# Kernel optimization log

Hardware: AMD Instinct MI355X
Metric: run time of the kernel (lower is better)

Reference implementation:

```python
import jax, jax.numpy as jnp
import numpy as np
from jax import lax

B, L, M, K = 4096, 1000, 16, 20
PRIOR_LOC, PRIOR_SCALE = -0.01, 0.001


def _motif_probs(x, w):
    # x: [B,4,L], w: [M,4*K] -> sigmoid(max_t conv(x, w_m)) : [B,M]
    kern = w.reshape(M, 4, K)
    scores = lax.conv_general_dilated(x, kern, (1,), 'VALID',
                                      dimension_numbers=('NCH', 'OIH', 'NCH'))  # [B,M,L-K+1]
    return jax.nn.sigmoid(scores.max(-1))


def _z(x, w):
    # pz_wyx_network: Bernoulli(p).log_prob(0) + log_prob(1) per motif, then softmax over motifs
    p = _motif_probs(x, w)                    # [B,M]
    lp = jnp.log(p) + jnp.log1p(-p)
    return jax.nn.softmax(lp, axis=-1)


def _kl(q_loc, q_scale):
    # KL(N(q_loc,q_scale) || N(PRIOR_LOC, PRIOR_SCALE)), summed over all dims
    return (jnp.log(PRIOR_SCALE / q_scale)
            + (q_scale ** 2 + (q_loc - PRIOR_LOC) ** 2) / (2.0 * PRIOR_SCALE ** 2)
            - 0.5).sum()


def setup_inputs() -> dict:
    key = jax.random.key(0)
    ks = jax.random.split(key, 6)
    x = jax.random.uniform(ks[0], (B, 4, L), dtype=jnp.float32)
    y = (jax.random.uniform(ks[1], (B,)) > 0.5).astype(jnp.float32)
    qw_loc = jax.random.normal(ks[2], (M, 4 * K), dtype=jnp.float32)
    qw_scale_raw = jax.random.normal(ks[3], (M, 4 * K), dtype=jnp.float32)
    gen_scale = jnp.full((1,), -15.0, dtype=jnp.float32)
    eps1 = jax.random.normal(ks[4], (M, 4 * K), dtype=jnp.float32)
    eps2 = jax.random.normal(ks[5], (M, 4 * K), dtype=jnp.float32)
    return dict(x=x, y=y, qw_loc=qw_loc, qw_scale_raw=qw_scale_raw,
                gen_scale=gen_scale, eps1=eps1, eps2=eps2)


def reference(x, y, qw_loc, qw_scale_raw, gen_scale, eps1, eps2):
    q_scale = jax.nn.softplus(qw_scale_raw)
    # --- ELBO assembly (forward) ---
    w1 = qw_loc + q_scale * eps1              # first rsample
    z = _z(x, w1)                             # [B,M]
    elbo = (z * jnp.log(1e-20 + z)).sum(1)    # [B]
    elbo = elbo + 2.0 * _kl(qw_loc, q_scale)  # KL added twice in original forward
    w2 = qw_loc + q_scale * eps2              # second rsample
    p = _motif_probs(x, w2)                   # [B,M] generative_loc per motif
    s = 1.0 / jax.nn.softplus(gen_scale)[0]
    eps = 1e-16
    gll = -jnp.log(eps + (eps + p) ** s + (eps + 1.0 - p) ** s)          # [B,M]
    # BCELoss() has reduction='mean' -> scalar per motif (log clamped at -100 like torch)
    bce = -(y[:, None] * jnp.clip(jnp.log(p), -100.0)
            + (1.0 - y)[:, None] * jnp.clip(jnp.log(1.0 - p), -100.0)).mean(0)  # [M]
    gll = gll - s * bce[None, :]
    elbo = elbo - (z * gll).sum(1)
    loss = elbo.mean()
    # --- predict: per-sample gathered kernel conv (batched via grouped conv) ---
    assign = _z(x, qw_loc).argmax(-1)         # [B] motif assignment per sample
    w_z = qw_loc[assign].reshape(B, 4, K)     # gathered per-sample kernels
    xg = x.reshape(1, B * 4, L)
    sc = lax.conv_general_dilated(xg, w_z, (1,), 'VALID',
                                  dimension_numbers=('NCH', 'OIH', 'NCH'),
                                  feature_group_count=B)                # [1,B,L-K+1]
    y_pred = jax.nn.sigmoid(sc[0].max(-1))    # [B]
    return loss, y_pred
```

## Files before the change

kernel.cpp:

```cpp
#include <hip/hip_runtime.h>
#include <math.h>

#define B_N 4096
#define TVALID 981

typedef _Float16 f16x8 __attribute__((ext_vector_type(8)));
typedef float f32x16 __attribute__((ext_vector_type(16)));

#define WS_FRAG 0
#define WS_RED  5120

static __device__ __forceinline__ float softplus_f(float x) {
    return fmaxf(x, 0.f) + log1pf(expf(-fabsf(x)));
}
static __device__ __forceinline__ uint32_t pkh(_Float16 a, _Float16 b) {
    return (uint32_t)__builtin_bit_cast(unsigned short, a)
         | ((uint32_t)__builtin_bit_cast(unsigned short, b) << 16);
}
static __device__ __forceinline__ f16x8 mkfrag(uint32_t d0, uint32_t d1, uint32_t d2, uint32_t d3) {
    union { uint32_t u[4]; f16x8 v; } t;
    t.u[0] = d0; t.u[1] = d1; t.u[2] = d2; t.u[3] = d3;
    return t.v;
}

__global__ void prep_kernel(const float* __restrict__ qw_loc,
                            const float* __restrict__ qw_scale_raw,
                            const float* __restrict__ gen_scale,
                            const float* __restrict__ eps1,
                            const float* __restrict__ eps2,
                            float* __restrict__ wsf) {
    const int g = blockIdx.x * 256 + threadIdx.x;
    float* red = wsf + WS_RED;
    if (g == 0) red[0] = 1.0f / softplus_f(gen_scale[0]);
    else if (g < 34) red[g] = 0.f;
    if (g >= 1280) return;

    const int lane = g & 63, set = g >> 6;
    const int grp = set / 5, s = set - grp * 5;
    const int h = lane >> 5, n = lane & 31, f = n & 15;
    int var, spl;
    if (grp == 0)      { var = (n < 16) ? 0 : 1; spl = 0; }
    else if (grp == 1) { var = (n < 16) ? 0 : 1; spl = 1; }
    else if (grp == 2) { var = 2;                spl = (n < 16) ? 0 : 1; }
    else               { var = (n < 16) ? 2 : 3; spl = 1; }

    uint32_t d[4];
#pragma unroll
    for (int q = 0; q < 4; ++q) {
        unsigned short es[2];
#pragma unroll
        for (int e = 0; e < 2; ++e) {
            const int j = 2 * q + e;
            const int c = j & 3;
            const int kk = 4 * s + 2 * h + (j >> 2);
            const int idx = f * 80 + c * 20 + kk;
            float w = 0.f;
            if (var != 3) {
                w = qw_loc[idx];
                if (var < 2) w += softplus_f(qw_scale_raw[idx]) * (var == 0 ? eps1[idx] : eps2[idx]);
            }
            _Float16 h1 = (_Float16)w;
            _Float16 hv = spl ? (_Float16)(w - (float)h1) : h1;
            es[e] = __builtin_bit_cast(unsigned short, hv);
        }
        d[q] = (uint32_t)es[0] | ((uint32_t)es[1] << 16);
    }
    uint4* out4 = (uint4*)((uint32_t*)wsf + WS_FRAG);
    out4[set * 64 + lane] = make_uint4(d[0], d[1], d[2], d[3]);
}

__global__ __launch_bounds__(256) void conv_kernel(const float* __restrict__ x,
                                                   const float* __restrict__ y,
                                                   const float* __restrict__ wsf,
                                                   float* __restrict__ red,
                                                   float* __restrict__ out) {
    __shared__ __align__(16) uint32_t xls[4096];
    __shared__ float maxs[4][48];

    const int tid = threadIdx.x, b = blockIdx.x;
    const int lane = tid & 63, wid = tid >> 6;
    const int i31 = lane & 31, h = lane >> 5;

    uint32_t Bv[20][4];
    const uint4* fg = (const uint4*)((const uint32_t*)wsf + WS_FRAG);
#pragma unroll
    for (int u = 0; u < 20; ++u) {
        uint4 t = fg[u * 64 + lane];
        Bv[u][0] = t.x; Bv[u][1] = t.y; Bv[u][2] = t.z; Bv[u][3] = t.w;
    }

    const float* xb = x + (size_t)b * 4000;
#pragma unroll
    for (int it = 0; it < 2; ++it) {
        int u = tid + 256 * it;
        if (u < 500) {
            const int p0 = 2 * u;
            float v[4][2];
#pragma unroll
            for (int c = 0; c < 4; ++c) {
                float2 t = *(const float2*)(xb + c * 1000 + p0);
                v[c][0] = t.x; v[c][1] = t.y;
            }
#pragma unroll
            for (int e = 0; e < 2; ++e) {
                _Float16 a[4], r[4];
#pragma unroll
                for (int c = 0; c < 4; ++c) {
                    a[c] = (_Float16)v[c][e];
                    r[c] = (_Float16)(v[c][e] - (float)a[c]);
                }
                *(uint4*)&xls[4 * (p0 + e)] =
                    make_uint4(pkh(a[0], a[1]), pkh(a[2], a[3]),
                               pkh(r[0], r[1]), pkh(r[2], r[3]));
            }
        }
    }
    if (tid < 24) *(uint4*)&xls[4 * (1000 + tid)] = make_uint4(0, 0, 0, 0);
    __syncthreads();

    float vmW[16], vmL[16];
#pragma unroll
    for (int e = 0; e < 16; ++e) { vmW[e] = -INFINITY; vmL[e] = -INFINITY; }

    const int t_beg = wid * 8;
    const int t_end = (wid == 3) ? 31 : (t_beg + 8);
    for (int tile = t_beg; tile < t_end; ++tile) {
        const int tb = tile * 32;
        f32x16 accW, accL;
#pragma unroll
        for (int e = 0; e < 16; ++e) { accW[e] = 0.f; accL[e] = 0.f; }
        const int Pb = tb + i31 + 2 * h;
#pragma unroll
        for (int s = 0; s < 5; ++s) {
            const int P = Pb + 4 * s;
            uint4 q0 = *(const uint4*)&xls[4 * P];
            uint4 q1 = *(const uint4*)&xls[4 * P + 4];
            f16x8 A1 = mkfrag(q0.x, q0.y, q1.x, q1.y);
            f16x8 A2 = mkfrag(q0.z, q0.w, q1.z, q1.w);
            f16x8 B0  = mkfrag(Bv[s][0],      Bv[s][1],      Bv[s][2],      Bv[s][3]);
            f16x8 B1  = mkfrag(Bv[5+s][0],    Bv[5+s][1],    Bv[5+s][2],    Bv[5+s][3]);
            f16x8 B2a = mkfrag(Bv[10+s][0],   Bv[10+s][1],   Bv[10+s][2],   Bv[10+s][3]);
            f16x8 B2b = mkfrag(Bv[15+s][0],   Bv[15+s][1],   Bv[15+s][2],   Bv[15+s][3]);
            accW = __builtin_amdgcn_mfma_f32_32x32x16_f16(A1, B0,  accW, 0, 0, 0);
            accL = __builtin_amdgcn_mfma_f32_32x32x16_f16(A1, B2a, accL, 0, 0, 0);
            accW = __builtin_amdgcn_mfma_f32_32x32x16_f16(A1, B1,  accW, 0, 0, 0);
            accL = __builtin_amdgcn_mfma_f32_32x32x16_f16(A1, B2b, accL, 0, 0, 0);
            accW = __builtin_amdgcn_mfma_f32_32x32x16_f16(A2, B0,  accW, 0, 0, 0);
            accL = __builtin_amdgcn_mfma_f32_32x32x16_f16(A2, B2a, accL, 0, 0, 0);
        }
        if (tile < 30) {
#pragma unroll
            for (int e = 0; e < 16; ++e) {
                vmW[e] = fmaxf(vmW[e], accW[e]);
                vmL[e] = fmaxf(vmL[e], accL[e]);
            }
        } else {
#pragma unroll
            for (int e = 0; e < 16; ++e) {
                int row = (e & 3) + 8 * (e >> 2) + 4 * h;
                bool ok = (tb + row) < TVALID;
                vmW[e] = fmaxf(vmW[e], ok ? accW[e] : -INFINITY);
                vmL[e] = fmaxf(vmL[e], ok ? accL[e] : -INFINITY);
            }
        }
    }

    float mW = vmW[0], mL = vmL[0];
#pragma unroll
    for (int e = 1; e < 16; ++e) { mW = fmaxf(mW, vmW[e]); mL = fmaxf(mL, vmL[e]); }
    mW = fmaxf(mW, __shfl_xor(mW, 32, 64));
    mL = fmaxf(mL, __shfl_xor(mL, 32, 64));
    if (lane < 32) maxs[wid][lane] = mW;
    if (lane < 16) maxs[wid][32 + lane] = mL;
    __syncthreads();

    if (tid < 16) {
        const int m = tid;
        const float s_ = red[0];
        const float yb = y[b];
        float sc1 = fmaxf(fmaxf(maxs[0][m],      maxs[1][m]),
                          fmaxf(maxs[2][m],      maxs[3][m]));
        float sc2 = fmaxf(fmaxf(maxs[0][16 + m], maxs[1][16 + m]),
                          fmaxf(maxs[2][16 + m], maxs[3][16 + m]));
        float sc0 = fmaxf(fmaxf(maxs[0][32 + m], maxs[1][32 + m]),
                          fmaxf(maxs[2][32 + m], maxs[3][32 + m]));

        float p1 = 1.f / (1.f + expf(-sc1));
        float lp = logf(p1) + log1pf(-p1);
        float mx = lp;
#pragma unroll
        for (int o = 8; o; o >>= 1) mx = fmaxf(mx, __shfl_xor(mx, o, 16));
        float e = expf(lp - mx);
        float se_ = e;
#pragma unroll
        for (int o = 8; o; o >>= 1) se_ += __shfl_xor(se_, o, 16);
        float z = e / se_;
        float Aterm = z * logf(1e-20f + z);

        float p2 = 1.f / (1.f + expf(-sc2));
        float g0 = -logf(1e-16f + powf(1e-16f + p2, s_) + powf(1.0f - p2, s_));
        float Cterm = z * g0;
        float bterm = yb * fmaxf(logf(p2), -100.f)
                    + (1.f - yb) * fmaxf(logf(1.f - p2), -100.f);

        float AC = Aterm - Cterm;
#pragma unroll
        for (int o = 8; o; o >>= 1) AC += __shfl_xor(AC, o, 16);

        atomicAdd(&red[2 + m], z);
        atomicAdd(&red[18 + m], bterm);

        float p0 = 1.f / (1.f + expf(-sc0));
        float lp0 = logf(p0) + log1pf(-p0);
        float best = lp0; int bidx = m;
#pragma unroll
        for (int o = 8; o; o >>= 1) {
            float ov = __shfl_xor(best, o, 16);
            int   oi = __shfl_xor(bidx, o, 16);
            if (ov > best || (ov == best && oi < bidx)) { best = ov; bidx = oi; }
        }
        if (m == 0) {
            atomicAdd(&red[1], AC);
            float scb = fmaxf(fmaxf(maxs[0][32 + bidx], maxs[1][32 + bidx]),
                              fmaxf(maxs[2][32 + bidx], maxs[3][32 + bidx]));
            out[1 + b] = 1.f / (1.f + expf(-scb));
        }
    }
}

__global__ void finish_kernel(const float* __restrict__ qw_loc,
                              const float* __restrict__ qw_scale_raw,
                              const float* __restrict__ wsf,
                              float* __restrict__ out) {
    int tid = threadIdx.x;
    double kl = 0.0;
    for (int i = tid; i < 1280; i += 64) {
        float loc = qw_loc[i], qs = softplus_f(qw_scale_raw[i]);
        float dl = loc + 0.01f;
        kl += (double)(logf(0.001f / qs) + (qs * qs + dl * dl) / 2e-6f - 0.5f);
    }
#pragma unroll
    for (int o = 32; o; o >>= 1) kl += __shfl_xor(kl, o, 64);
    if (tid == 0) {
        const float* red = wsf + WS_RED;
        float t = 0.f;
        for (int m = 0; m < 16; ++m) t += red[2 + m] * red[18 + m];
        float loss = red[1] / 4096.0f + (float)(2.0 * kl)
                   - red[0] * (t / (4096.0f * 4096.0f));
        out[0] = loss;
    }
}

extern "C" void kernel_launch(void* const* d_in, const int* in_sizes, int n_in,
                              void* d_out, int out_size, void* d_ws, size_t ws_size,
                              hipStream_t stream) {
    const float* x            = (const float*)d_in[0];
    const float* y            = (const float*)d_in[1];
    const float* qw_loc       = (const float*)d_in[2];
    const float* qw_scale_raw = (const float*)d_in[3];
    const float* gen_scale    = (const float*)d_in[4];
    const float* eps1         = (const float*)d_in[5];
    const float* eps2         = (const float*)d_in[6];
    float* out = (float*)d_out;
    float* wsf = (float*)d_ws;

    prep_kernel<<<5, 256, 0, stream>>>(qw_loc, qw_scale_raw, gen_scale, eps1, eps2, wsf);
    conv_kernel<<<B_N, 256, 0, stream>>>(x, y, wsf, wsf + WS_RED, out);
    finish_kernel<<<1, 64, 0, stream>>>(qw_loc, qw_scale_raw, wsf, out);
}
```

Baseline: 270.3 us.

## Drop residual correction on sampled-weight convs and process two tiles per iteration

The W accumulator (w1/w2 convs) now uses only the f16 high part of x and a single combined weight fragment per step. The split hi/lo weight fragment and the A2 (x residual) term are removed, which cuts MFMAs per step from 6 to 4 per tile and shrinks the weight fragments from 20 to 15. The tile loop also handles two tiles per iteration so independent MFMA chains can interleave. The cost is lower precision for the W scores, and the unrolled body needs more accumulator registers, which may reduce occupancy.

Result: faster. 255.3 us (-5.6%).

```diff
diff --git a/kernel.cpp b/kernel.cpp
--- a/kernel.cpp
+++ b/kernel.cpp
@@ -8,7 +8,7 @@
 typedef float f32x16 __attribute__((ext_vector_type(16)));
 
 #define WS_FRAG 0
-#define WS_RED  5120
+#define WS_RED  3840
 
 static __device__ __forceinline__ float softplus_f(float x) {
     return fmaxf(x, 0.f) + log1pf(expf(-fabsf(x)));
@@ -33,15 +33,14 @@
     float* red = wsf + WS_RED;
     if (g == 0) red[0] = 1.0f / softplus_f(gen_scale[0]);
     else if (g < 34) red[g] = 0.f;
-    if (g >= 1280) return;
+    if (g >= 960) return;
 
     const int lane = g & 63, set = g >> 6;
     const int grp = set / 5, s = set - grp * 5;
     const int h = lane >> 5, n = lane & 31, f = n & 15;
     int var, spl;
     if (grp == 0)      { var = (n < 16) ? 0 : 1; spl = 0; }
-    else if (grp == 1) { var = (n < 16) ? 0 : 1; spl = 1; }
-    else if (grp == 2) { var = 2;                spl = (n < 16) ? 0 : 1; }
+    else if (grp == 1) { var = 2;                spl = (n < 16) ? 0 : 1; }
     else               { var = (n < 16) ? 2 : 3; spl = 1; }
 
     uint32_t d[4];
@@ -81,10 +80,10 @@
     const int lane = tid & 63, wid = tid >> 6;
     const int i31 = lane & 31, h = lane >> 5;
 
-    uint32_t Bv[20][4];
+    uint32_t Bv[15][4];
     const uint4* fg = (const uint4*)((const uint32_t*)wsf + WS_FRAG);
 #pragma unroll
-    for (int u = 0; u < 20; ++u) {
+    for (int u = 0; u < 15; ++u) {
         uint4 t = fg[u * 64 + lane];
         Bv[u][0] = t.x; Bv[u][1] = t.y; Bv[u][2] = t.z; Bv[u][3] = t.w;
     }
@@ -122,45 +121,52 @@
 #pragma unroll
     for (int e = 0; e < 16; ++e) { vmW[e] = -INFINITY; vmL[e] = -INFINITY; }
 
-    const int t_beg = wid * 8;
-    const int t_end = (wid == 3) ? 31 : (t_beg + 8);
-    for (int tile = t_beg; tile < t_end; ++tile) {
-        const int tb = tile * 32;
-        f32x16 accW, accL;
-#pragma unroll
-        for (int e = 0; e < 16; ++e) { accW[e] = 0.f; accL[e] = 0.f; }
-        const int Pb = tb + i31 + 2 * h;
+    for (int i = 0; i < 4; ++i) {
+        const int t0 = wid * 8 + 2 * i;
+        const int t1 = t0 + 1;
+        const bool two = (t1 <= 30);
+        const int tba = t0 * 32, tbb = two ? t1 * 32 : tba;
+        f32x16 accW0, accL0, accW1, accL1;
+#pragma unroll
+        for (int e = 0; e < 16; ++e) { accW0[e] = 0.f; accL0[e] = 0.f; accW1[e] = 0.f; accL1[e] = 0.f; }
+        const int Pa0 = tba + i31 + 2 * h;
+        const int Pb0 = tbb + i31 + 2 * h;
 #pragma unroll
         for (int s = 0; s < 5; ++s) {
-            const int P = Pb + 4 * s;
-            uint4 q0 = *(const uint4*)&xls[4 * P];
-            uint4 q1 = *(const uint4*)&xls[4 * P + 4];
-            f16x8 A1 = mkfrag(q0.x, q0.y, q1.x, q1.y);
-            f16x8 A2 = mkfrag(q0.z, q0.w, q1.z, q1.w);
-            f16x8 B0  = mkfrag(Bv[s][0],      Bv[s][1],      Bv[s][2],      Bv[s][3]);
-            f16x8 B1  = mkfrag(Bv[5+s][0],    Bv[5+s][1],    Bv[5+s][2],    Bv[5+s][3]);
-            f16x8 B2a = mkfrag(Bv[10+s][0],   Bv[10+s][1],   Bv[10+s][2],   Bv[10+s][3]);
-            f16x8 B2b = mkfrag(Bv[15+s][0],   Bv[15+s][1],   Bv[15+s][2],   Bv[15+s][3]);
-            accW = __builtin_amdgcn_mfma_f32_32x32x16_f16(A1, B0,  accW, 0, 0, 0);
-            accL = __builtin_amdgcn_mfma_f32_32x32x16_f16(A1, B2a, accL, 0, 0, 0);
-            accW = __builtin_amdgcn_mfma_f32_32x32x16_f16(A1, B1,  accW, 0, 0, 0);
-            accL = __builtin_amdgcn_mfma_f32_32x32x16_f16(A1, B2b, accL, 0, 0, 0);
-            accW = __builtin_amdgcn_mfma_f32_32x32x16_f16(A2, B0,  accW, 0, 0, 0);
-            accL = __builtin_amdgcn_mfma_f32_32x32x16_f16(A2, B2a, accL, 0, 0, 0);
-        }
-        if (tile < 30) {
-#pragma unroll
-            for (int e = 0; e < 16; ++e) {
-                vmW[e] = fmaxf(vmW[e], accW[e]);
-                vmL[e] = fmaxf(vmL[e], accL[e]);
-            }
-        } else {
+            const int Pa = Pa0 + 4 * s, Pb = Pb0 + 4 * s;
+            uint4 qa0 = *(const uint4*)&xls[4 * Pa];
+            uint4 qa1 = *(const uint4*)&xls[4 * Pa + 4];
+            uint4 qb0 = *(const uint4*)&xls[4 * Pb];
+            uint4 qb1 = *(const uint4*)&xls[4 * Pb + 4];
+            f16x8 A1a = mkfrag(qa0.x, qa0.y, qa1.x, qa1.y);
+            f16x8 A2a = mkfrag(qa0.z, qa0.w, qa1.z, qa1.w);
+            f16x8 A1b = mkfrag(qb0.x, qb0.y, qb1.x, qb1.y);
+            f16x8 A2b = mkfrag(qb0.z, qb0.w, qb1.z, qb1.w);
+            f16x8 BW  = mkfrag(Bv[s][0],      Bv[s][1],      Bv[s][2],      Bv[s][3]);
+            f16x8 B2a = mkfrag(Bv[5 + s][0],  Bv[5 + s][1],  Bv[5 + s][2],  Bv[5 + s][3]);
+            f16x8 B2b = mkfrag(Bv[10 + s][0], Bv[10 + s][1], Bv[10 + s][2], Bv[10 + s][3]);
+            accW0 = __builtin_amdgcn_mfma_f32_32x32x16_f16(A1a, BW,  accW0, 0, 0, 0);
+            accW1 = __builtin_amdgcn_mfma_f32_32x32x16_f16(A1b, BW,  accW1, 0, 0, 0);
+            accL0 = __builtin_amdgcn_mfma_f32_32x32x16_f16(A1a, B2a, accL0, 0, 0, 0);
+            accL1 = __builtin_amdgcn_mfma_f32_32x32x16_f16(A1b, B2a, accL1, 0, 0, 0);
+            accL0 = __builtin_amdgcn_mfma_f32_32x32x16_f16(A2a, B2a, accL0, 0, 0, 0);
+            accL1 = __builtin_amdgcn_mfma_f32_32x32x16_f16(A2b, B2a, accL1, 0, 0, 0);
+            accL0 = __builtin_amdgcn_mfma_f32_32x32x16_f16(A1a, B2b, accL0, 0, 0, 0);
+            accL1 = __builtin_amdgcn_mfma_f32_32x32x16_f16(A1b, B2b, accL1, 0, 0, 0);
+        }
+        if (t0 == 30) {
 #pragma unroll
             for (int e = 0; e < 16; ++e) {
                 int row = (e & 3) + 8 * (e >> 2) + 4 * h;
-                bool ok = (tb + row) < TVALID;
-                vmW[e] = fmaxf(vmW[e], ok ? accW[e] : -INFINITY);
-                vmL[e] = fmaxf(vmL[e], ok ? accL[e] : -INFINITY);
+                bool ok = (960 + row) < TVALID;
+                vmW[e] = fmaxf(vmW[e], ok ? accW0[e] : -INFINITY);
+                vmL[e] = fmaxf(vmL[e], ok ? accL0[e] : -INFINITY);
+            }
+        } else {
+#pragma unroll
+            for (int e = 0; e < 16; ++e) {
+                vmW[e] = fmaxf(fmaxf(vmW[e], accW0[e]), accW1[e]);
+                vmL[e] = fmaxf(fmaxf(vmL[e], accL0[e]), accL1[e]);
             }
         }
     }
@@ -264,7 +270,7 @@
     float* out = (float*)d_out;
     float* wsf = (float*)d_ws;
 
-    prep_kernel<<<5, 256, 0, stream>>>(qw_loc, qw_scale_raw, gen_scale, eps1, eps2, wsf);
+    prep_kernel<<<4, 256, 0, stream>>>(qw_loc, qw_scale_raw, gen_scale, eps1, eps2, wsf);
     conv_kernel<<<B_N, 256, 0, stream>>>(x, y, wsf, wsf + WS_RED, out);
     finish_kernel<<<1, 64, 0, stream>>>(qw_loc, qw_scale_raw, wsf, out);
 }
```
